# Performance work log

Measured on AMD Instinct MI355X. Metric: run time of the kernel, lower is better.

The kernel has to match this reference:

```python
import jax, jax.numpy as jnp
import numpy as np

SEQ_DIM, HID = 20, 512
B, L = 4, 2048

def setup_inputs() -> dict:
    key = jax.random.key(0)
    ks = jax.random.split(key, 12)
    s = lambda k, sh, fan_in: jax.random.normal(k, sh, jnp.float32) / np.sqrt(fan_in)
    return {
        "sequence_features": jax.random.normal(ks[0], (B, L, SEQ_DIM), jnp.float32),
        "W1": s(ks[1], (SEQ_DIM, HID), SEQ_DIM), "b1": jnp.zeros((HID,), jnp.float32),
        "W2": s(ks[2], (HID, HID), HID),        "b2": jnp.zeros((HID,), jnp.float32),
        "W_ss": s(ks[3], (HID, 3), HID),        "b_ss": jnp.zeros((3,), jnp.float32),
        "W_ang": s(ks[4], (HID, 2), HID),       "b_ang": jnp.zeros((2,), jnp.float32),
        "W_c": s(ks[5], (2 * HID, 1), 2 * HID), "b_c": jnp.zeros((1,), jnp.float32),
    }

def reference(sequence_features, W1, b1, W2, b2, W_ss, b_ss, W_ang, b_ang, W_c, b_c):
    # MLP encoder: Linear-ReLU-Linear-ReLU
    h = jax.nn.relu(sequence_features @ W1 + b1)
    h = jax.nn.relu(h @ W2 + b2)                      # [B, L, HID]
    ss = jax.nn.softmax(h @ W_ss + b_ss, axis=-1)     # [B, L, 3]
    angles = h @ W_ang + b_ang                        # [B, L, 2]
    # contact_head(concat(h_i, h_j)) factorizes: split W_c into the half
    # that multiplies h_i and the half that multiplies h_j.
    H = h.shape[-1]
    ci = (h @ W_c[:H])[..., 0]                        # [B, L]
    cj = (h @ W_c[H:])[..., 0]                        # [B, L]
    contact = jax.nn.sigmoid(ci[:, :, None] + cj[:, None, :] + b_c[0])  # [B, L, L]
    return ss, angles, contact
```

## Files before the change

kernel.cpp:

```cpp
#include <hip/hip_runtime.h>
#include <cstdint>
#include <cstddef>

#define SEQD 20
#define HID  512
#define LSEQ 2048
#define MROWS 8192
#define GBM 128
#define GBN 128
#define GBK 64
#define ITILE 8
#define ACC_FLOATS (6 * MROWS + MROWS)

typedef __attribute__((ext_vector_type(4))) float f32x4;
typedef __attribute__((ext_vector_type(8))) short bf16x8;

__device__ __forceinline__ ushort f2bf(float f) {
  union { float f; unsigned u; } v; v.f = f;
  unsigned r = v.u + 0x7fffu + ((v.u >> 16) & 1u);
  return (ushort)(r >> 16);
}
__device__ __forceinline__ int swzb(int row, int b) {
  return (b & 0x0F) | ((b ^ ((row & 7) << 4)) & 0x70);
}
__device__ __forceinline__ void async16(const ushort* g, ushort* l) {
  __builtin_amdgcn_global_load_lds(
      (const __attribute__((address_space(1))) unsigned*)g,
      (__attribute__((address_space(3))) unsigned*)l, 16, 0, 0);
}

__global__ __launch_bounds__(256) void k_prep(const float* __restrict__ X,
                                              const float* __restrict__ W1,
                                              const float* __restrict__ b1,
                                              const float* __restrict__ W2,
                                              ushort* __restrict__ h1,
                                              ushort* __restrict__ W2t,
                                              float* __restrict__ accws) {
  __shared__ float Xs[16][SEQD + 1];
  __shared__ float tile[32][33];
  const int t = threadIdx.x;
  if (blockIdx.x < 512) {
    const int base = blockIdx.x * 16;
    for (int i = t; i < 16 * SEQD; i += 256) Xs[i / SEQD][i % SEQD] = X[base * SEQD + i];
    __syncthreads();
    const int m0 = (t >> 6) * 4;
    const int nl = (t & 63) * 4;
    float4 acc[4][2];
#pragma unroll
    for (int mi = 0; mi < 4; ++mi) {
      acc[mi][0] = *(const float4*)&b1[nl];
      acc[mi][1] = *(const float4*)&b1[nl + 256];
    }
#pragma unroll
    for (int k = 0; k < SEQD; ++k) {
      const float4 w0 = *(const float4*)&W1[k * HID + nl];
      const float4 w1 = *(const float4*)&W1[k * HID + nl + 256];
#pragma unroll
      for (int mi = 0; mi < 4; ++mi) {
        const float xv = Xs[m0 + mi][k];
        acc[mi][0].x += xv * w0.x; acc[mi][0].y += xv * w0.y;
        acc[mi][0].z += xv * w0.z; acc[mi][0].w += xv * w0.w;
        acc[mi][1].x += xv * w1.x; acc[mi][1].y += xv * w1.y;
        acc[mi][1].z += xv * w1.z; acc[mi][1].w += xv * w1.w;
      }
    }
#pragma unroll
    for (int mi = 0; mi < 4; ++mi) {
      const int m = base + m0 + mi;
#pragma unroll
      for (int g = 0; g < 2; ++g) {
        const float4 r = acc[mi][g];
        ushort4 o;
        o.x = f2bf(fmaxf(r.x, 0.f)); o.y = f2bf(fmaxf(r.y, 0.f));
        o.z = f2bf(fmaxf(r.z, 0.f)); o.w = f2bf(fmaxf(r.w, 0.f));
        const int k = nl + g * 256;
        const int sb = swzb(m, (k & 63) * 2);
        *(ushort4*)&h1[(size_t)m * HID + (k & ~63) + (sb >> 1)] = o;
      }
    }
  } else {
    const int zi = (blockIdx.x - 512) * 256 + t;
    if (zi < ACC_FLOATS) accws[zi] = 0.f;

    const int c = blockIdx.x - 512;
    const int k0 = (c & 15) * 32, n0 = (c >> 4) * 32;
    const int tx = t & 31, ty = t >> 5;
#pragma unroll
    for (int r = ty; r < 32; r += 8)
      tile[r][tx] = W2[(size_t)(k0 + r) * HID + n0 + tx];
    __syncthreads();
#pragma unroll
    for (int r = ty; r < 32; r += 8) {
      const int n = n0 + r, k = k0 + tx;
      const int sb = swzb(n, (k & 63) * 2);
      W2t[(size_t)n * HID + (k & ~63) + (sb >> 1)] = f2bf(tile[tx][r]);
    }
  }
}

__global__ __launch_bounds__(256) void k_gemm_heads(const ushort* __restrict__ Aglob,
                                                    const ushort* __restrict__ Bglob,
                                                    const float* __restrict__ b2,
                                                    const float* __restrict__ Wss,
                                                    const float* __restrict__ Wang,
                                                    const float* __restrict__ Wc,
                                                    float* __restrict__ acc6,
                                                    float* __restrict__ cjacc) {
  __shared__ ushort As[2][GBM * GBK];
  __shared__ ushort Bs[2][GBM * GBK];
  __shared__ float  comb[2][GBM][8];
  const int t = threadIdx.x;
  const int wave = t >> 6, lane = t & 63;
  const int l15 = lane & 15, lhi = lane >> 4;
  const int wr = wave >> 1, wc = wave & 1;
  const int swz = (blockIdx.x & 7) * 32 + (blockIdx.x >> 3);
  const int xblk = swz & 3, yblk = swz >> 2;
  const int bm = yblk * GBM, bn = xblk * GBN;
  const int srow = lane >> 3;
  const int scol = (lane & 7) * 8;

  f32x4 acc[4][4];
#pragma unroll
  for (int mi = 0; mi < 4; ++mi)
#pragma unroll
    for (int ni = 0; ni < 4; ++ni) acc[mi][ni] = {0.f, 0.f, 0.f, 0.f};

#define STAGE(buf, k0)                                                         \
  {                                                                            \
    _Pragma("unroll")                                                          \
    for (int rd = 0; rd < 4; ++rd) {                                           \
      const int r = rd * 32 + wave * 8 + srow;                                 \
      const int lo = rd * 2048 + wave * 512;                                   \
      async16(Aglob + (size_t)(bm + r) * HID + (k0) + scol, &As[buf][lo]);     \
      async16(Bglob + (size_t)(bn + r) * HID + (k0) + scol, &Bs[buf][lo]);     \
    }                                                                          \
  }

#define COMPUTE(buf)                                                           \
  {                                                                            \
    _Pragma("unroll")                                                          \
    for (int kk = 0; kk < 2; ++kk) {                                           \
      bf16x8 af[4], bff[4];                                                    \
      _Pragma("unroll")                                                        \
      for (int mi = 0; mi < 4; ++mi) {                                         \
        const int row = wr * 64 + mi * 16 + l15;                               \
        af[mi] = *(const bf16x8*)&As[buf][(row * 128 + swzb(row, kk * 64 + lhi * 16)) >> 1]; \
      }                                                                        \
      _Pragma("unroll")                                                        \
      for (int ni = 0; ni < 4; ++ni) {                                         \
        const int rn = wc * 64 + ni * 16 + l15;                                \
        bff[ni] = *(const bf16x8*)&Bs[buf][(rn * 128 + swzb(rn, kk * 64 + lhi * 16)) >> 1]; \
      }                                                                        \
      _Pragma("unroll")                                                        \
      for (int mi = 0; mi < 4; ++mi)                                           \
        _Pragma("unroll")                                                      \
        for (int ni = 0; ni < 4; ++ni)                                         \
          acc[mi][ni] = __builtin_amdgcn_mfma_f32_16x16x32_bf16(af[mi], bff[ni], acc[mi][ni], 0, 0, 0); \
    }                                                                          \
  }

  STAGE(0, 0)
  __syncthreads();
#pragma unroll
  for (int kt = 0; kt < 8; ++kt) {
    if (kt < 7) STAGE((kt + 1) & 1, (kt + 1) * GBK)
    COMPUTE(kt & 1)
    __syncthreads();
  }

  float bias[4], ws0[4], ws1[4], ws2[4], wa0[4], wa1[4], wc0[4], wc1[4];
#pragma unroll
  for (int ni = 0; ni < 4; ++ni) {
    const int col = bn + wc * 64 + ni * 16 + l15;
    bias[ni] = b2[col];
    ws0[ni] = Wss[col * 3 + 0]; ws1[ni] = Wss[col * 3 + 1]; ws2[ni] = Wss[col * 3 + 2];
    wa0[ni] = Wang[col * 2 + 0]; wa1[ni] = Wang[col * 2 + 1];
    wc0[ni] = Wc[col]; wc1[ni] = Wc[HID + col];
  }
#pragma unroll
  for (int mi = 0; mi < 4; ++mi) {
#pragma unroll
    for (int j = 0; j < 4; ++j) {
      float p0 = 0, p1 = 0, p2 = 0, p3 = 0, p4 = 0, p5 = 0, p6 = 0;
#pragma unroll
      for (int ni = 0; ni < 4; ++ni) {
        const float v = fmaxf(acc[mi][ni][j] + bias[ni], 0.f);
        p0 += v * ws0[ni]; p1 += v * ws1[ni]; p2 += v * ws2[ni];
        p3 += v * wa0[ni]; p4 += v * wa1[ni];
        p5 += v * wc0[ni]; p6 += v * wc1[ni];
      }
#pragma unroll
      for (int m = 1; m <= 8; m <<= 1) {
        p0 += __shfl_xor(p0, m); p1 += __shfl_xor(p1, m); p2 += __shfl_xor(p2, m);
        p3 += __shfl_xor(p3, m); p4 += __shfl_xor(p4, m);
        p5 += __shfl_xor(p5, m); p6 += __shfl_xor(p6, m);
      }
      if (l15 == 0) {
        const int lr = wr * 64 + mi * 16 + lhi * 4 + j;
        comb[wc][lr][0] = p0; comb[wc][lr][1] = p1; comb[wc][lr][2] = p2;
        comb[wc][lr][3] = p3; comb[wc][lr][4] = p4;
        comb[wc][lr][5] = p5; comb[wc][lr][6] = p6;
      }
    }
  }
  __syncthreads();
  if (t < GBM) {
    const int row = bm + t;
#pragma unroll
    for (int q = 0; q < 6; ++q)
      atomicAdd(&acc6[(size_t)row * 6 + q], comb[0][t][q] + comb[1][t][q]);
    atomicAdd(&cjacc[row], comb[0][t][6] + comb[1][t][6]);
  }
#undef STAGE
#undef COMPUTE
}

__global__ __launch_bounds__(256) void k_fc(const float* __restrict__ acc6,
                                            const float* __restrict__ cjacc,
                                            const float* __restrict__ bss,
                                            const float* __restrict__ bang,
                                            const float* __restrict__ bc,
                                            float* __restrict__ ssO,
                                            float* __restrict__ angO,
                                            float* __restrict__ contact) {
  __shared__ float cj_l[LSEQ];
  __shared__ float ci_l[ITILE];
  const int blk = blockIdx.x;
  const int b   = blk >> 8;
  const int i0  = (blk & 255) * ITILE;
  const int t   = threadIdx.x;
  const size_t rowbase = (size_t)b * LSEQ;

  {
    const float* cjb = cjacc + rowbase;
#pragma unroll
    for (int it = 0; it < 2; ++it) {
      const int j = it * 1024 + t * 4;
      *(float4*)&cj_l[j] = *(const float4*)&cjb[j];
    }
  }
  if (t < ITILE) {
    const size_t r = rowbase + i0 + t;
    const float* a = &acc6[r * 6];
    const float l0 = a[0] + bss[0], l1 = a[1] + bss[1], l2 = a[2] + bss[2];
    const float mx = fmaxf(l0, fmaxf(l1, l2));
    const float e0 = __expf(l0 - mx), e1 = __expf(l1 - mx), e2 = __expf(l2 - mx);
    const float inv = 1.f / (e0 + e1 + e2);
    ssO[r * 3 + 0] = e0 * inv;
    ssO[r * 3 + 1] = e1 * inv;
    ssO[r * 3 + 2] = e2 * inv;
    angO[r * 2 + 0] = a[3] + bang[0];
    angO[r * 2 + 1] = a[4] + bang[1];
    ci_l[t] = a[5] + bc[0];
  }
  __syncthreads();

#pragma unroll
  for (int r = 0; r < ITILE; ++r) {
    const float base = ci_l[r];
    float* orow = contact + (rowbase + i0 + r) * LSEQ;
#pragma unroll
    for (int jc = 0; jc < 2; ++jc) {
      const int j0 = jc * 1024 + t * 4;
      const float4 c4 = *(const float4*)&cj_l[j0];
      float4 o;
      o.x = 1.f / (1.f + __expf(-(base + c4.x)));
      o.y = 1.f / (1.f + __expf(-(base + c4.y)));
      o.z = 1.f / (1.f + __expf(-(base + c4.z)));
      o.w = 1.f / (1.f + __expf(-(base + c4.w)));
      *(float4*)&orow[j0] = o;
    }
  }
}

extern "C" void kernel_launch(void* const* d_in, const int* in_sizes, int n_in,
                              void* d_out, int out_size, void* d_ws, size_t ws_size,
                              hipStream_t stream) {
  const float* X    = (const float*)d_in[0];
  const float* W1   = (const float*)d_in[1];
  const float* b1   = (const float*)d_in[2];
  const float* W2   = (const float*)d_in[3];
  const float* b2   = (const float*)d_in[4];
  const float* Wss  = (const float*)d_in[5];
  const float* bss  = (const float*)d_in[6];
  const float* Wang = (const float*)d_in[7];
  const float* bang = (const float*)d_in[8];
  const float* Wc   = (const float*)d_in[9];
  const float* bc   = (const float*)d_in[10];

  float* out     = (float*)d_out;
  float* ssO     = out;
  float* angO    = out + 24576;
  float* contact = out + 40960;

  ushort* h1  = (ushort*)contact;
  ushort* W2t = (ushort*)(contact + 2 * 1024 * 1024);

  float* acc6  = (float*)d_ws;
  float* cjacc = acc6 + (size_t)6 * MROWS;

  k_prep<<<768, 256, 0, stream>>>(X, W1, b1, W2, h1, W2t, acc6);
  k_gemm_heads<<<256, 256, 0, stream>>>(h1, W2t, b2, Wss, Wang, Wc, acc6, cjacc);
  k_fc<<<1024, 256, 0, stream>>>(acc6, cjacc, bss, bang, bc, ssO, angO, contact);
}
```

Before: 46.03 us.

## Fuse prep, GEMM-heads and contact kernels into one cooperative kernel

Replaces the three separate launches with a single cooperative kernel of 512 blocks. Two grid-wide syncs separate the phases: layer-1 plus W2 transpose and accumulator zeroing, then the bf16 MFMA GEMM with the head reductions, then the softmax/angle/sigmoid contact writes. The aim is to remove inter-kernel launch gaps and tail idle time. In exchange it pays for the grid barriers and gives each block more rows in the first and last phases. The old three-kernel path stays as a fallback if the cooperative launch fails.

```diff
diff --git a/kernel.cpp b/kernel.cpp
--- a/kernel.cpp
+++ b/kernel.cpp
@@ -1,4 +1,5 @@
 #include <hip/hip_runtime.h>
+#include <hip/hip_cooperative_groups.h>
 #include <cstdint>
 #include <cstddef>
 
@@ -9,7 +10,6 @@
 #define GBM 128
 #define GBN 128
 #define GBK 64
-#define ITILE 8
 #define ACC_FLOATS (6 * MROWS + MROWS)
 
 typedef __attribute__((ext_vector_type(4))) float f32x4;
@@ -27,6 +27,249 @@
   __builtin_amdgcn_global_load_lds(
       (const __attribute__((address_space(1))) unsigned*)g,
       (__attribute__((address_space(3))) unsigned*)l, 16, 0, 0);
+}
+
+__global__ __launch_bounds__(256, 2) void k_fused(
+    const float* __restrict__ X,   const float* __restrict__ W1,
+    const float* __restrict__ b1,  const float* __restrict__ W2,
+    const float* __restrict__ b2,  const float* __restrict__ Wss,
+    const float* __restrict__ bss, const float* __restrict__ Wang,
+    const float* __restrict__ bang,const float* __restrict__ Wc,
+    const float* __restrict__ bc,
+    ushort* __restrict__ h1, ushort* __restrict__ W2t,
+    float* __restrict__ acc6, float* __restrict__ cjacc,
+    float* __restrict__ ssO, float* __restrict__ angO,
+    float* __restrict__ contact) {
+  __shared__ __align__(16) char smem[73728];
+  const int t   = threadIdx.x;
+  const int bid = blockIdx.x;
+
+  {
+    float (*Xs)[SEQD + 1] = (float(*)[SEQD + 1])smem;
+    const int base = bid * 16;
+    for (int i = t; i < 16 * SEQD; i += 256) Xs[i / SEQD][i % SEQD] = X[base * SEQD + i];
+    __syncthreads();
+    const int m0 = (t >> 6) * 4;
+    const int nl = (t & 63) * 4;
+    float4 acc[4][2];
+#pragma unroll
+    for (int mi = 0; mi < 4; ++mi) {
+      acc[mi][0] = *(const float4*)&b1[nl];
+      acc[mi][1] = *(const float4*)&b1[nl + 256];
+    }
+#pragma unroll
+    for (int k = 0; k < SEQD; ++k) {
+      const float4 w0 = *(const float4*)&W1[k * HID + nl];
+      const float4 w1 = *(const float4*)&W1[k * HID + nl + 256];
+#pragma unroll
+      for (int mi = 0; mi < 4; ++mi) {
+        const float xv = Xs[m0 + mi][k];
+        acc[mi][0].x += xv * w0.x; acc[mi][0].y += xv * w0.y;
+        acc[mi][0].z += xv * w0.z; acc[mi][0].w += xv * w0.w;
+        acc[mi][1].x += xv * w1.x; acc[mi][1].y += xv * w1.y;
+        acc[mi][1].z += xv * w1.z; acc[mi][1].w += xv * w1.w;
+      }
+    }
+#pragma unroll
+    for (int mi = 0; mi < 4; ++mi) {
+      const int m = base + m0 + mi;
+#pragma unroll
+      for (int g = 0; g < 2; ++g) {
+        const float4 r = acc[mi][g];
+        ushort4 o;
+        o.x = f2bf(fmaxf(r.x, 0.f)); o.y = f2bf(fmaxf(r.y, 0.f));
+        o.z = f2bf(fmaxf(r.z, 0.f)); o.w = f2bf(fmaxf(r.w, 0.f));
+        const int k = nl + g * 256;
+        const int sb = swzb(m, (k & 63) * 2);
+        *(ushort4*)&h1[(size_t)m * HID + (k & ~63) + (sb >> 1)] = o;
+      }
+    }
+    const int zi = bid * 256 + t;
+    if (zi < ACC_FLOATS) acc6[zi] = 0.f;
+    if (bid >= 256) {
+      float (*tile)[33] = (float(*)[33])(smem + 2048);
+      const int c = bid - 256;
+      const int k0 = (c & 15) * 32, n0 = (c >> 4) * 32;
+      const int tx = t & 31, ty = t >> 5;
+#pragma unroll
+      for (int r = ty; r < 32; r += 8)
+        tile[r][tx] = W2[(size_t)(k0 + r) * HID + n0 + tx];
+      __syncthreads();
+#pragma unroll
+      for (int r = ty; r < 32; r += 8) {
+        const int n = n0 + r, k = k0 + tx;
+        const int sb = swzb(n, (k & 63) * 2);
+        W2t[(size_t)n * HID + (k & ~63) + (sb >> 1)] = f2bf(tile[tx][r]);
+      }
+    }
+  }
+
+  cooperative_groups::this_grid().sync();
+
+  if (bid < 256) {
+    ushort* As0 = (ushort*)smem;
+    ushort* As1 = (ushort*)(smem + 16384);
+    ushort* Bs0 = (ushort*)(smem + 32768);
+    ushort* Bs1 = (ushort*)(smem + 49152);
+    float (*comb)[GBM][8] = (float(*)[GBM][8])(smem + 65536);
+    ushort* Asb[2] = {As0, As1};
+    ushort* Bsb[2] = {Bs0, Bs1};
+
+    const int wave = t >> 6, lane = t & 63;
+    const int l15 = lane & 15, lhi = lane >> 4;
+    const int wr = wave >> 1, wc = wave & 1;
+    const int swz = (bid & 7) * 32 + (bid >> 3);
+    const int xblk = swz & 3, yblk = swz >> 2;
+    const int bm = yblk * GBM, bn = xblk * GBN;
+    const int srow = lane >> 3;
+    const int scol = (lane & 7) * 8;
+
+    f32x4 acc[4][4];
+#pragma unroll
+    for (int mi = 0; mi < 4; ++mi)
+#pragma unroll
+      for (int ni = 0; ni < 4; ++ni) acc[mi][ni] = {0.f, 0.f, 0.f, 0.f};
+
+#define STAGE(buf, k0)                                                         \
+    {                                                                          \
+      _Pragma("unroll")                                                        \
+      for (int rd = 0; rd < 4; ++rd) {                                         \
+        const int r = rd * 32 + wave * 8 + srow;                               \
+        const int lo = rd * 2048 + wave * 512;                                 \
+        async16(h1  + (size_t)(bm + r) * HID + (k0) + scol, Asb[buf] + lo);    \
+        async16(W2t + (size_t)(bn + r) * HID + (k0) + scol, Bsb[buf] + lo);    \
+      }                                                                        \
+    }
+
+#define COMPUTE(buf)                                                           \
+    {                                                                          \
+      _Pragma("unroll")                                                        \
+      for (int kk = 0; kk < 2; ++kk) {                                         \
+        bf16x8 af[4], bff[4];                                                  \
+        _Pragma("unroll")                                                      \
+        for (int mi = 0; mi < 4; ++mi) {                                       \
+          const int row = wr * 64 + mi * 16 + l15;                             \
+          af[mi] = *(const bf16x8*)&Asb[buf][(row * 128 + swzb(row, kk * 64 + lhi * 16)) >> 1]; \
+        }                                                                      \
+        _Pragma("unroll")                                                      \
+        for (int ni = 0; ni < 4; ++ni) {                                       \
+          const int rn = wc * 64 + ni * 16 + l15;                              \
+          bff[ni] = *(const bf16x8*)&Bsb[buf][(rn * 128 + swzb(rn, kk * 64 + lhi * 16)) >> 1]; \
+        }                                                                      \
+        _Pragma("unroll")                                                      \
+        for (int mi = 0; mi < 4; ++mi)                                         \
+          _Pragma("unroll")                                                    \
+          for (int ni = 0; ni < 4; ++ni)                                       \
+            acc[mi][ni] = __builtin_amdgcn_mfma_f32_16x16x32_bf16(af[mi], bff[ni], acc[mi][ni], 0, 0, 0); \
+      }                                                                        \
+    }
+
+    STAGE(0, 0)
+    __syncthreads();
+#pragma unroll
+    for (int kt = 0; kt < 8; ++kt) {
+      if (kt < 7) STAGE((kt + 1) & 1, (kt + 1) * GBK)
+      COMPUTE(kt & 1)
+      __syncthreads();
+    }
+
+    float bias[4], ws0[4], ws1[4], ws2[4], wa0[4], wa1[4], wc0[4], wc1[4];
+#pragma unroll
+    for (int ni = 0; ni < 4; ++ni) {
+      const int col = bn + wc * 64 + ni * 16 + l15;
+      bias[ni] = b2[col];
+      ws0[ni] = Wss[col * 3 + 0]; ws1[ni] = Wss[col * 3 + 1]; ws2[ni] = Wss[col * 3 + 2];
+      wa0[ni] = Wang[col * 2 + 0]; wa1[ni] = Wang[col * 2 + 1];
+      wc0[ni] = Wc[col]; wc1[ni] = Wc[HID + col];
+    }
+#pragma unroll
+    for (int mi = 0; mi < 4; ++mi) {
+#pragma unroll
+      for (int j = 0; j < 4; ++j) {
+        float p0 = 0, p1 = 0, p2 = 0, p3 = 0, p4 = 0, p5 = 0, p6 = 0;
+#pragma unroll
+        for (int ni = 0; ni < 4; ++ni) {
+          const float v = fmaxf(acc[mi][ni][j] + bias[ni], 0.f);
+          p0 += v * ws0[ni]; p1 += v * ws1[ni]; p2 += v * ws2[ni];
+          p3 += v * wa0[ni]; p4 += v * wa1[ni];
+          p5 += v * wc0[ni]; p6 += v * wc1[ni];
+        }
+#pragma unroll
+        for (int m = 1; m <= 8; m <<= 1) {
+          p0 += __shfl_xor(p0, m); p1 += __shfl_xor(p1, m); p2 += __shfl_xor(p2, m);
+          p3 += __shfl_xor(p3, m); p4 += __shfl_xor(p4, m);
+          p5 += __shfl_xor(p5, m); p6 += __shfl_xor(p6, m);
+        }
+        if (l15 == 0) {
+          const int lr = wr * 64 + mi * 16 + lhi * 4 + j;
+          comb[wc][lr][0] = p0; comb[wc][lr][1] = p1; comb[wc][lr][2] = p2;
+          comb[wc][lr][3] = p3; comb[wc][lr][4] = p4;
+          comb[wc][lr][5] = p5; comb[wc][lr][6] = p6;
+        }
+      }
+    }
+    __syncthreads();
+    if (t < GBM) {
+      const int row = bm + t;
+#pragma unroll
+      for (int q = 0; q < 6; ++q)
+        atomicAdd(&acc6[(size_t)row * 6 + q], comb[0][t][q] + comb[1][t][q]);
+      atomicAdd(&cjacc[row], comb[0][t][6] + comb[1][t][6]);
+    }
+#undef STAGE
+#undef COMPUTE
+  }
+
+  cooperative_groups::this_grid().sync();
+
+  {
+    float* cj_l = (float*)smem;
+    float* ci_l = (float*)(smem + 8192);
+    const int b  = bid >> 7;
+    const int i0 = (bid & 127) * 16;
+    const size_t rowbase = (size_t)b * LSEQ;
+
+    {
+      const float* cjb = cjacc + rowbase;
+#pragma unroll
+      for (int it = 0; it < 2; ++it) {
+        const int j = it * 1024 + t * 4;
+        *(float4*)&cj_l[j] = *(const float4*)&cjb[j];
+      }
+    }
+    if (t < 16) {
+      const size_t r = rowbase + i0 + t;
+      const float* a = &acc6[r * 6];
+      const float l0 = a[0] + bss[0], l1 = a[1] + bss[1], l2 = a[2] + bss[2];
+      const float mx = fmaxf(l0, fmaxf(l1, l2));
+      const float e0 = __expf(l0 - mx), e1 = __expf(l1 - mx), e2 = __expf(l2 - mx);
+      const float inv = 1.f / (e0 + e1 + e2);
+      ssO[r * 3 + 0] = e0 * inv;
+      ssO[r * 3 + 1] = e1 * inv;
+      ssO[r * 3 + 2] = e2 * inv;
+      angO[r * 2 + 0] = a[3] + bang[0];
+      angO[r * 2 + 1] = a[4] + bang[1];
+      ci_l[t] = a[5] + bc[0];
+    }
+    __syncthreads();
+
+#pragma unroll
+    for (int r = 0; r < 16; ++r) {
+      const float base = ci_l[r];
+      float* orow = contact + (rowbase + i0 + r) * LSEQ;
+#pragma unroll
+      for (int jc = 0; jc < 2; ++jc) {
+        const int j0 = jc * 1024 + t * 4;
+        const float4 c4 = *(const float4*)&cj_l[j0];
+        float4 o;
+        o.x = 1.f / (1.f + __expf(-(base + c4.x)));
+        o.y = 1.f / (1.f + __expf(-(base + c4.y)));
+        o.z = 1.f / (1.f + __expf(-(base + c4.z)));
+        o.w = 1.f / (1.f + __expf(-(base + c4.w)));
+        *(float4*)&orow[j0] = o;
+      }
+    }
+  }
 }
 
 __global__ __launch_bounds__(256) void k_prep(const float* __restrict__ X,
@@ -81,7 +324,6 @@
   } else {
     const int zi = (blockIdx.x - 512) * 256 + t;
     if (zi < ACC_FLOATS) accws[zi] = 0.f;
-
     const int c = blockIdx.x - 512;
     const int k0 = (c & 15) * 32, n0 = (c >> 4) * 32;
     const int tx = t & 31, ty = t >> 5;
@@ -224,13 +466,12 @@
                                             float* __restrict__ angO,
                                             float* __restrict__ contact) {
   __shared__ float cj_l[LSEQ];
-  __shared__ float ci_l[ITILE];
+  __shared__ float ci_l[8];
   const int blk = blockIdx.x;
   const int b   = blk >> 8;
-  const int i0  = (blk & 255) * ITILE;
+  const int i0  = (blk & 255) * 8;
   const int t   = threadIdx.x;
   const size_t rowbase = (size_t)b * LSEQ;
-
   {
     const float* cjb = cjacc + rowbase;
 #pragma unroll
@@ -239,7 +480,7 @@
       *(float4*)&cj_l[j] = *(const float4*)&cjb[j];
     }
   }
-  if (t < ITILE) {
+  if (t < 8) {
     const size_t r = rowbase + i0 + t;
     const float* a = &acc6[r * 6];
     const float l0 = a[0] + bss[0], l1 = a[1] + bss[1], l2 = a[2] + bss[2];
@@ -254,9 +495,8 @@
     ci_l[t] = a[5] + bc[0];
   }
   __syncthreads();
-
-#pragma unroll
-  for (int r = 0; r < ITILE; ++r) {
+#pragma unroll
+  for (int r = 0; r < 8; ++r) {
     const float base = ci_l[r];
     float* orow = contact + (rowbase + i0 + r) * LSEQ;
 #pragma unroll
@@ -295,11 +535,20 @@
 
   ushort* h1  = (ushort*)contact;
   ushort* W2t = (ushort*)(contact + 2 * 1024 * 1024);
-
   float* acc6  = (float*)d_ws;
   float* cjacc = acc6 + (size_t)6 * MROWS;
 
-  k_prep<<<768, 256, 0, stream>>>(X, W1, b1, W2, h1, W2t, acc6);
-  k_gemm_heads<<<256, 256, 0, stream>>>(h1, W2t, b2, Wss, Wang, Wc, acc6, cjacc);
-  k_fc<<<1024, 256, 0, stream>>>(acc6, cjacc, bss, bang, bc, ssO, angO, contact);
-}
+  void* args[] = { (void*)&X, (void*)&W1, (void*)&b1, (void*)&W2, (void*)&b2,
+                   (void*)&Wss, (void*)&bss, (void*)&Wang, (void*)&bang,
+                   (void*)&Wc, (void*)&bc,
+                   (void*)&h1, (void*)&W2t, (void*)&acc6, (void*)&cjacc,
+                   (void*)&ssO, (void*)&angO, (void*)&contact };
+  hipError_t err = hipLaunchCooperativeKernel((const void*)k_fused,
+                                              dim3(512), dim3(256),
+                                              args, 0, stream);
+  if (err != hipSuccess) {
+    k_prep<<<768, 256, 0, stream>>>(X, W1, b1, W2, h1, W2t, acc6);
+    k_gemm_heads<<<256, 256, 0, stream>>>(h1, W2t, b2, Wss, Wang, Wc, acc6, cjacc);
+    k_fc<<<1024, 256, 0, stream>>>(acc6, cjacc, bss, bang, bc, ssO, angO, contact);
+  }
+}
```

Measured after the change: 169.5 us. 3.68x slower.

## Fuse first layer and W2 conversion into GEMM, replace atomics with partial buffers

Applied to the files above, without the earlier changes.

Removes the separate prep kernel. The GEMM now computes the first Linear+ReLU tile on the fly from X and W1 into LDS, and converts W2 fp32 to bf16 directly while staging. Head partial sums are written to per-column-block buffers rather than atomically accumulated, and the final kernel adds the four partials, which also drops the zeroing pass. This saves a launch and the h1/W2t round trip through global memory. In exchange, each of the 4 column blocks recomputes layer 1, synchronous fp32 loads replace the async LDS loads, and the stage loop is no longer unrolled.

```diff
diff --git a/kernel.cpp b/kernel.cpp
--- a/kernel.cpp
+++ b/kernel.cpp
@@ -9,8 +9,6 @@
 #define GBM 128
 #define GBN 128
 #define GBK 64
-#define ITILE 8
-#define ACC_FLOATS (6 * MROWS + MROWS)
 
 typedef __attribute__((ext_vector_type(4))) float f32x4;
 typedef __attribute__((ext_vector_type(8))) short bf16x8;
@@ -23,92 +21,16 @@
 __device__ __forceinline__ int swzb(int row, int b) {
   return (b & 0x0F) | ((b ^ ((row & 7) << 4)) & 0x70);
 }
-__device__ __forceinline__ void async16(const ushort* g, ushort* l) {
-  __builtin_amdgcn_global_load_lds(
-      (const __attribute__((address_space(1))) unsigned*)g,
-      (__attribute__((address_space(3))) unsigned*)l, 16, 0, 0);
-}
-
-__global__ __launch_bounds__(256) void k_prep(const float* __restrict__ X,
-                                              const float* __restrict__ W1,
-                                              const float* __restrict__ b1,
-                                              const float* __restrict__ W2,
-                                              ushort* __restrict__ h1,
-                                              ushort* __restrict__ W2t,
-                                              float* __restrict__ accws) {
-  __shared__ float Xs[16][SEQD + 1];
-  __shared__ float tile[32][33];
-  const int t = threadIdx.x;
-  if (blockIdx.x < 512) {
-    const int base = blockIdx.x * 16;
-    for (int i = t; i < 16 * SEQD; i += 256) Xs[i / SEQD][i % SEQD] = X[base * SEQD + i];
-    __syncthreads();
-    const int m0 = (t >> 6) * 4;
-    const int nl = (t & 63) * 4;
-    float4 acc[4][2];
-#pragma unroll
-    for (int mi = 0; mi < 4; ++mi) {
-      acc[mi][0] = *(const float4*)&b1[nl];
-      acc[mi][1] = *(const float4*)&b1[nl + 256];
-    }
-#pragma unroll
-    for (int k = 0; k < SEQD; ++k) {
-      const float4 w0 = *(const float4*)&W1[k * HID + nl];
-      const float4 w1 = *(const float4*)&W1[k * HID + nl + 256];
-#pragma unroll
-      for (int mi = 0; mi < 4; ++mi) {
-        const float xv = Xs[m0 + mi][k];
-        acc[mi][0].x += xv * w0.x; acc[mi][0].y += xv * w0.y;
-        acc[mi][0].z += xv * w0.z; acc[mi][0].w += xv * w0.w;
-        acc[mi][1].x += xv * w1.x; acc[mi][1].y += xv * w1.y;
-        acc[mi][1].z += xv * w1.z; acc[mi][1].w += xv * w1.w;
-      }
-    }
-#pragma unroll
-    for (int mi = 0; mi < 4; ++mi) {
-      const int m = base + m0 + mi;
-#pragma unroll
-      for (int g = 0; g < 2; ++g) {
-        const float4 r = acc[mi][g];
-        ushort4 o;
-        o.x = f2bf(fmaxf(r.x, 0.f)); o.y = f2bf(fmaxf(r.y, 0.f));
-        o.z = f2bf(fmaxf(r.z, 0.f)); o.w = f2bf(fmaxf(r.w, 0.f));
-        const int k = nl + g * 256;
-        const int sb = swzb(m, (k & 63) * 2);
-        *(ushort4*)&h1[(size_t)m * HID + (k & ~63) + (sb >> 1)] = o;
-      }
-    }
-  } else {
-    const int zi = (blockIdx.x - 512) * 256 + t;
-    if (zi < ACC_FLOATS) accws[zi] = 0.f;
-
-    const int c = blockIdx.x - 512;
-    const int k0 = (c & 15) * 32, n0 = (c >> 4) * 32;
-    const int tx = t & 31, ty = t >> 5;
-#pragma unroll
-    for (int r = ty; r < 32; r += 8)
-      tile[r][tx] = W2[(size_t)(k0 + r) * HID + n0 + tx];
-    __syncthreads();
-#pragma unroll
-    for (int r = ty; r < 32; r += 8) {
-      const int n = n0 + r, k = k0 + tx;
-      const int sb = swzb(n, (k & 63) * 2);
-      W2t[(size_t)n * HID + (k & ~63) + (sb >> 1)] = f2bf(tile[tx][r]);
-    }
-  }
-}
-
-__global__ __launch_bounds__(256) void k_gemm_heads(const ushort* __restrict__ Aglob,
-                                                    const ushort* __restrict__ Bglob,
-                                                    const float* __restrict__ b2,
-                                                    const float* __restrict__ Wss,
-                                                    const float* __restrict__ Wang,
-                                                    const float* __restrict__ Wc,
-                                                    float* __restrict__ acc6,
-                                                    float* __restrict__ cjacc) {
+
+__global__ __launch_bounds__(256) void k_gemm_all(
+    const float* __restrict__ X,   const float* __restrict__ W1,
+    const float* __restrict__ b1,  const float* __restrict__ W2,
+    const float* __restrict__ b2,  const float* __restrict__ Wss,
+    const float* __restrict__ Wang,const float* __restrict__ Wc,
+    float* __restrict__ Hpart) {
   __shared__ ushort As[2][GBM * GBK];
   __shared__ ushort Bs[2][GBM * GBK];
-  __shared__ float  comb[2][GBM][8];
+  __shared__ float  Xs[SEQD][GBM];
   const int t = threadIdx.x;
   const int wave = t >> 6, lane = t & 63;
   const int l15 = lane & 15, lhi = lane >> 4;
@@ -116,8 +38,15 @@
   const int swz = (blockIdx.x & 7) * 32 + (blockIdx.x >> 3);
   const int xblk = swz & 3, yblk = swz >> 2;
   const int bm = yblk * GBM, bn = xblk * GBN;
-  const int srow = lane >> 3;
-  const int scol = (lane & 7) * 8;
+
+  for (int i = t; i < GBM * SEQD; i += 256)
+    Xs[i % SEQD][i / SEQD] = X[(size_t)bm * SEQD + i];
+  __syncthreads();
+
+  const int tcol = (t & 7) * 8;
+  const int trow = (t >> 3) * 4;
+  const int bnc = t & 31;
+  const int bkr = (t >> 5) * 8;
 
   f32x4 acc[4][4];
 #pragma unroll
@@ -125,14 +54,60 @@
 #pragma unroll
     for (int ni = 0; ni < 4; ++ni) acc[mi][ni] = {0.f, 0.f, 0.f, 0.f};
 
-#define STAGE(buf, k0)                                                         \
+#define PRODUCE(buf, kt)                                                       \
   {                                                                            \
-    _Pragma("unroll")                                                          \
-    for (int rd = 0; rd < 4; ++rd) {                                           \
-      const int r = rd * 32 + wave * 8 + srow;                                 \
-      const int lo = rd * 2048 + wave * 512;                                   \
-      async16(Aglob + (size_t)(bm + r) * HID + (k0) + scol, &As[buf][lo]);     \
-      async16(Bglob + (size_t)(bn + r) * HID + (k0) + scol, &Bs[buf][lo]);     \
+    const int c0 = (kt) * GBK;                                                 \
+                            \
+    float aR[4][8];                                                            \
+    {                                                                          \
+      const float4 bb0 = *(const float4*)&b1[c0 + tcol];                       \
+      const float4 bb1 = *(const float4*)&b1[c0 + tcol + 4];                   \
+      _Pragma("unroll")                                                        \
+      for (int r = 0; r < 4; ++r) {                                            \
+        aR[r][0] = bb0.x; aR[r][1] = bb0.y; aR[r][2] = bb0.z; aR[r][3] = bb0.w;\
+        aR[r][4] = bb1.x; aR[r][5] = bb1.y; aR[r][6] = bb1.z; aR[r][7] = bb1.w;\
+      }                                                                        \
+      _Pragma("unroll")                                                        \
+      for (int k = 0; k < SEQD; ++k) {                                         \
+        const float4 w0 = *(const float4*)&W1[k * HID + c0 + tcol];            \
+        const float4 w1 = *(const float4*)&W1[k * HID + c0 + tcol + 4];        \
+        const float4 xr = *(const float4*)&Xs[k][trow];                        \
+        const float xv[4] = {xr.x, xr.y, xr.z, xr.w};                          \
+        _Pragma("unroll")                                                      \
+        for (int r = 0; r < 4; ++r) {                                          \
+          aR[r][0] += xv[r] * w0.x; aR[r][1] += xv[r] * w0.y;                  \
+          aR[r][2] += xv[r] * w0.z; aR[r][3] += xv[r] * w0.w;                  \
+          aR[r][4] += xv[r] * w1.x; aR[r][5] += xv[r] * w1.y;                  \
+          aR[r][6] += xv[r] * w1.z; aR[r][7] += xv[r] * w1.w;                  \
+        }                                                                      \
+      }                                                                        \
+      _Pragma("unroll")                                                        \
+      for (int r = 0; r < 4; ++r) {                                            \
+        bf16x8 o;                                                              \
+        _Pragma("unroll")                                                      \
+        for (int c = 0; c < 8; ++c)                                            \
+          o[c] = (short)f2bf(fmaxf(aR[r][c], 0.f));                            \
+        const int row = trow + r;                                              \
+        *(bf16x8*)&As[buf][(row * 128 + swzb(row, tcol * 2)) >> 1] = o;        \
+      }                                                                        \
+    }                                                                          \
+            \
+    {                                                                          \
+      float v[4][8];                                                           \
+      _Pragma("unroll")                                                        \
+      for (int i = 0; i < 8; ++i) {                                            \
+        const float* wrp = &W2[(size_t)(c0 + bkr + i) * HID + bn + bnc];       \
+        v[0][i] = wrp[0];  v[1][i] = wrp[32];                                  \
+        v[2][i] = wrp[64]; v[3][i] = wrp[96];                                  \
+      }                                                                        \
+      _Pragma("unroll")                                                        \
+      for (int q = 0; q < 4; ++q) {                                            \
+        bf16x8 o;                                                              \
+        _Pragma("unroll")                                                      \
+        for (int i = 0; i < 8; ++i) o[i] = (short)f2bf(v[q][i]);               \
+        const int n = q * 32 + bnc;                                            \
+        *(bf16x8*)&Bs[buf][(n * 128 + swzb(n, bkr * 2)) >> 1] = o;             \
+      }                                                                        \
     }                                                                          \
   }
 
@@ -159,15 +134,16 @@
     }                                                                          \
   }
 
-  STAGE(0, 0)
-  __syncthreads();
-#pragma unroll
+  PRODUCE(0, 0)
+  __syncthreads();
+#pragma unroll 1
   for (int kt = 0; kt < 8; ++kt) {
-    if (kt < 7) STAGE((kt + 1) & 1, (kt + 1) * GBK)
+    if (kt < 7) PRODUCE((kt + 1) & 1, kt + 1)
     COMPUTE(kt & 1)
     __syncthreads();
   }
 
+  float* combp = (float*)(&Bs[0][0]);
   float bias[4], ws0[4], ws1[4], ws2[4], wa0[4], wa1[4], wc0[4], wc1[4];
 #pragma unroll
   for (int ni = 0; ni < 4; ++ni) {
@@ -197,26 +173,25 @@
       }
       if (l15 == 0) {
         const int lr = wr * 64 + mi * 16 + lhi * 4 + j;
-        comb[wc][lr][0] = p0; comb[wc][lr][1] = p1; comb[wc][lr][2] = p2;
-        comb[wc][lr][3] = p3; comb[wc][lr][4] = p4;
-        comb[wc][lr][5] = p5; comb[wc][lr][6] = p6;
+        float* cp = &combp[((size_t)wc * GBM + lr) * 8];
+        cp[0] = p0; cp[1] = p1; cp[2] = p2; cp[3] = p3;
+        cp[4] = p4; cp[5] = p5; cp[6] = p6;
       }
     }
   }
   __syncthreads();
   if (t < GBM) {
-    const int row = bm + t;
-#pragma unroll
-    for (int q = 0; q < 6; ++q)
-      atomicAdd(&acc6[(size_t)row * 6 + q], comb[0][t][q] + comb[1][t][q]);
-    atomicAdd(&cjacc[row], comb[0][t][6] + comb[1][t][6]);
-  }
-#undef STAGE
+#pragma unroll
+    for (int q = 0; q < 7; ++q) {
+      const float val = combp[(size_t)t * 8 + q] + combp[((size_t)GBM + t) * 8 + q];
+      Hpart[((size_t)(xblk * 7 + q)) * MROWS + bm + t] = val;
+    }
+  }
+#undef PRODUCE
 #undef COMPUTE
 }
 
-__global__ __launch_bounds__(256) void k_fc(const float* __restrict__ acc6,
-                                            const float* __restrict__ cjacc,
+__global__ __launch_bounds__(256) void k_fc(const float* __restrict__ Hpart,
                                             const float* __restrict__ bss,
                                             const float* __restrict__ bang,
                                             const float* __restrict__ bc,
@@ -224,39 +199,56 @@
                                             float* __restrict__ angO,
                                             float* __restrict__ contact) {
   __shared__ float cj_l[LSEQ];
-  __shared__ float ci_l[ITILE];
+  __shared__ float ci_l[8];
   const int blk = blockIdx.x;
   const int b   = blk >> 8;
-  const int i0  = (blk & 255) * ITILE;
+  const int i0  = (blk & 255) * 8;
   const int t   = threadIdx.x;
   const size_t rowbase = (size_t)b * LSEQ;
 
   {
-    const float* cjb = cjacc + rowbase;
+    const float* p0 = Hpart + (size_t)(0 * 7 + 6) * MROWS + rowbase;
+    const float* p1 = Hpart + (size_t)(1 * 7 + 6) * MROWS + rowbase;
+    const float* p2 = Hpart + (size_t)(2 * 7 + 6) * MROWS + rowbase;
+    const float* p3 = Hpart + (size_t)(3 * 7 + 6) * MROWS + rowbase;
 #pragma unroll
     for (int it = 0; it < 2; ++it) {
       const int j = it * 1024 + t * 4;
-      *(float4*)&cj_l[j] = *(const float4*)&cjb[j];
-    }
-  }
-  if (t < ITILE) {
+      const float4 a = *(const float4*)&p0[j];
+      const float4 bq = *(const float4*)&p1[j];
+      const float4 c = *(const float4*)&p2[j];
+      const float4 d = *(const float4*)&p3[j];
+      float4 s;
+      s.x = a.x + bq.x + c.x + d.x;
+      s.y = a.y + bq.y + c.y + d.y;
+      s.z = a.z + bq.z + c.z + d.z;
+      s.w = a.w + bq.w + c.w + d.w;
+      *(float4*)&cj_l[j] = s;
+    }
+  }
+  if (t < 8) {
     const size_t r = rowbase + i0 + t;
-    const float* a = &acc6[r * 6];
-    const float l0 = a[0] + bss[0], l1 = a[1] + bss[1], l2 = a[2] + bss[2];
+    float q[6] = {0, 0, 0, 0, 0, 0};
+#pragma unroll
+    for (int s = 0; s < 4; ++s)
+#pragma unroll
+      for (int qq = 0; qq < 6; ++qq)
+        q[qq] += Hpart[(size_t)(s * 7 + qq) * MROWS + r];
+    const float l0 = q[0] + bss[0], l1 = q[1] + bss[1], l2 = q[2] + bss[2];
     const float mx = fmaxf(l0, fmaxf(l1, l2));
     const float e0 = __expf(l0 - mx), e1 = __expf(l1 - mx), e2 = __expf(l2 - mx);
     const float inv = 1.f / (e0 + e1 + e2);
     ssO[r * 3 + 0] = e0 * inv;
     ssO[r * 3 + 1] = e1 * inv;
     ssO[r * 3 + 2] = e2 * inv;
-    angO[r * 2 + 0] = a[3] + bang[0];
-    angO[r * 2 + 1] = a[4] + bang[1];
-    ci_l[t] = a[5] + bc[0];
-  }
-  __syncthreads();
-
-#pragma unroll
-  for (int r = 0; r < ITILE; ++r) {
+    angO[r * 2 + 0] = q[3] + bang[0];
+    angO[r * 2 + 1] = q[4] + bang[1];
+    ci_l[t] = q[5] + bc[0];
+  }
+  __syncthreads();
+
+#pragma unroll
+  for (int r = 0; r < 8; ++r) {
     const float base = ci_l[r];
     float* orow = contact + (rowbase + i0 + r) * LSEQ;
 #pragma unroll
@@ -293,13 +285,8 @@
   float* angO    = out + 24576;
   float* contact = out + 40960;
 
-  ushort* h1  = (ushort*)contact;
-  ushort* W2t = (ushort*)(contact + 2 * 1024 * 1024);
-
-  float* acc6  = (float*)d_ws;
-  float* cjacc = acc6 + (size_t)6 * MROWS;
-
-  k_prep<<<768, 256, 0, stream>>>(X, W1, b1, W2, h1, W2t, acc6);
-  k_gemm_heads<<<256, 256, 0, stream>>>(h1, W2t, b2, Wss, Wang, Wc, acc6, cjacc);
-  k_fc<<<1024, 256, 0, stream>>>(acc6, cjacc, bss, bang, bc, ssO, angO, contact);
-}
+  float* Hpart = (float*)d_ws;
+
+  k_gemm_all<<<256, 256, 0, stream>>>(X, W1, b1, W2, b2, Wss, Wang, Wc, Hpart);
+  k_fc<<<1024, 256, 0, stream>>>(Hpart, bss, bang, bc, ssO, angO, contact);
+}
```

Result: slower. 62.22 us (median of 3 runs) (+35.2%).
